# Optimization experiments

Measured on AMD Instinct MI355X. Metric: run time of the kernel, lower is better.

## Reference

```python
import jax, jax.numpy as jnp
import numpy as np

NUM_NODES = 100000
NUM_EDGES = 3200000
NUM_GRAPHS = 512
IN_DIM, OUT_DIM = 128, 16
DIMS = [IN_DIM, 32, 48, 64]


def glorot(key, shape):
    lim = float(np.sqrt(6.0 / (shape[0] + shape[1])))
    return jax.random.uniform(key, shape, jnp.float32, -lim, lim)


def setup_inputs() -> dict:
    key = jax.random.key(0)
    ks = jax.random.split(key, 12)
    x = jax.random.normal(ks[0], (NUM_NODES, IN_DIM), jnp.float32)
    edge_index = jax.random.randint(ks[1], (2, NUM_EDGES), 0, NUM_NODES, jnp.int64)
    batch = jnp.sort(jax.random.randint(ks[2], (NUM_NODES,), 0, NUM_GRAPHS, jnp.int64))
    params = {}
    for i in range(3):
        params[f"W{i+1}"] = glorot(ks[3 + i], (DIMS[i], DIMS[i + 1]))
        params[f"b{i+1}"] = jnp.zeros((DIMS[i + 1],), jnp.float32)
    params["fc1_w"] = glorot(ks[6], (64, 32))
    params["fc1_b"] = jnp.zeros((32,), jnp.float32)
    params["fc2_w"] = glorot(ks[7], (32, OUT_DIM))
    params["fc2_b"] = jnp.zeros((OUT_DIM,), jnp.float32)
    return {"x": x, "edge_index": edge_index, "batch": batch, **params}


def gcn_conv(x, W, b, src, dst, deg_inv_sqrt):
    # h = x @ W; aggregate with symmetric normalization + self loops (PyG GCNConv)
    h = x @ W  # [N, out]
    norm = deg_inv_sqrt[src] * deg_inv_sqrt[dst]  # [E]
    msg = h[src] * norm[:, None]  # [E, out]  (gather)
    agg = jnp.zeros_like(h).at[dst].add(msg)  # scatter-add to targets
    self_loop = h * (deg_inv_sqrt * deg_inv_sqrt)[:, None]
    return agg + self_loop + b


def reference(x, edge_index, batch, W1, b1, W2, b2, W3, b3, fc1_w, fc1_b, fc2_w, fc2_b):
    src, dst = edge_index[0], edge_index[1]
    n = x.shape[0]
    # degree with self loops: deg[i] = in-degree + 1
    deg = jnp.zeros((n,), jnp.float32).at[dst].add(1.0) + 1.0
    dis = jax.lax.rsqrt(deg)
    h = jax.nn.relu(gcn_conv(x, W1, b1, src, dst, dis))
    h = jax.nn.relu(gcn_conv(h, W2, b2, src, dst, dis))
    h = jax.nn.relu(gcn_conv(h, W3, b3, src, dst, dis))
    # global mean pool per graph
    sums = jax.ops.segment_sum(h, batch, num_segments=NUM_GRAPHS)
    cnts = jax.ops.segment_sum(jnp.ones((n,), jnp.float32), batch, num_segments=NUM_GRAPHS)
    pooled = sums / jnp.maximum(cnts, 1.0)[:, None]  # [G, 64]
    z = jax.nn.relu(pooled @ fc1_w + fc1_b)
    logits = z @ fc2_w + fc2_b
    return jax.nn.softmax(logits, axis=1)
```

## Files before the change

### kernel.cpp

```cpp
#include <hip/hip_runtime.h>
#include <hip/hip_fp16.h>

static constexpr int NN = 100000;
static constexpr int NE = 3200000;
static constexpr int NG = 512;
static constexpr int NCB = 196;
static constexpr int CHK = 8192;
static constexpr int NCH = (NE + CHK - 1) / CHK;
static constexpr int NCNT = NCB * NCH;
static constexpr int SCAN_BLK = 2048;
static constexpr int NSB = (NCNT + SCAN_BLK - 1) / SCAN_BLK;

typedef float f32x2 __attribute__((ext_vector_type(2)));

__device__ __forceinline__ void acc_fp8x4(unsigned v, float* a) {
    f32x2 lo = __builtin_amdgcn_cvt_pk_f32_fp8((int)v, false);
    f32x2 hi = __builtin_amdgcn_cvt_pk_f32_fp8((int)v, true);
    a[0] += lo.x; a[1] += lo.y; a[2] += hi.x; a[3] += hi.y;
}
__device__ __forceinline__ void set_fp8x4(unsigned v, float* a) {
    f32x2 lo = __builtin_amdgcn_cvt_pk_f32_fp8((int)v, false);
    f32x2 hi = __builtin_amdgcn_cvt_pk_f32_fp8((int)v, true);
    a[0] = lo.x; a[1] = lo.y; a[2] = hi.x; a[3] = hi.y;
}
__device__ __forceinline__ unsigned pack_fp8x4(float a, float b, float c, float d) {
    int p = __builtin_amdgcn_cvt_pk_fp8_f32(a, b, 0, false);
    p = __builtin_amdgcn_cvt_pk_fp8_f32(c, d, p, true);
    return (unsigned)p;
}

__global__ __launch_bounds__(256) void k_histC(const int4* __restrict__ dst4,
                                               int* __restrict__ cntC, int e4) {
    __shared__ int h[NCB];
    for (int i = threadIdx.x; i < NCB; i += 256) h[i] = 0;
    __syncthreads();
    const int s4 = blockIdx.x * (CHK / 4), e4end = min(s4 + CHK / 4, e4);
    for (int i = s4 + threadIdx.x; i < e4end; i += 256) {
        int4 d = dst4[i];
        atomicAdd(&h[d.x >> 9], 1);
        atomicAdd(&h[d.y >> 9], 1);
        atomicAdd(&h[d.z >> 9], 1);
        atomicAdd(&h[d.w >> 9], 1);
    }
    __syncthreads();
    for (int i = threadIdx.x; i < NCB; i += 256)
        cntC[(size_t)i * NCH + blockIdx.x] = h[i];
}

__global__ __launch_bounds__(256) void k_scanA(const int* __restrict__ in,
                                               int* __restrict__ out,
                                               int* __restrict__ bsum, int n) {
    __shared__ int s[256];
    const int tid = threadIdx.x;
    const int base = blockIdx.x * SCAN_BLK + tid * 8;
    int v[8], t = 0;
#pragma unroll
    for (int c = 0; c < 8; c++) {
        int idx = base + c;
        v[c] = (idx < n) ? in[idx] : 0;
        t += v[c];
    }
    s[tid] = t;
    __syncthreads();
    for (int off = 1; off < 256; off <<= 1) {
        int x = (tid >= off) ? s[tid - off] : 0;
        __syncthreads();
        s[tid] += x;
        __syncthreads();
    }
    if (tid == 255) bsum[blockIdx.x] = s[255];
    int run = s[tid] - t;
#pragma unroll
    for (int c = 0; c < 8; c++) {
        int idx = base + c;
        if (idx < n) out[idx] = run;
        run += v[c];
    }
}

__global__ __launch_bounds__(256) void k_scanB(int* __restrict__ bsum, int nb) {
    __shared__ int s[256];
    const int tid = threadIdx.x;
    int v = (tid < nb) ? bsum[tid] : 0;
    s[tid] = v;
    __syncthreads();
    for (int off = 1; off < 256; off <<= 1) {
        int x = (tid >= off) ? s[tid - off] : 0;
        __syncthreads();
        s[tid] += x;
        __syncthreads();
    }
    if (tid < nb) bsum[tid] = s[tid] - v;
}

__global__ __launch_bounds__(256) void k_scatC(const int4* __restrict__ src4,
                                               const int4* __restrict__ dst4,
                                               const int* __restrict__ sc,
                                               const int* __restrict__ bsum,
                                               unsigned* __restrict__ tmp, int e4) {
    __shared__ int cur[NCB];
    for (int i = threadIdx.x; i < NCB; i += 256) {
        size_t idx = (size_t)i * NCH + blockIdx.x;
        cur[i] = sc[idx] + bsum[idx >> 11];
    }
    __syncthreads();
    const int s4 = blockIdx.x * (CHK / 4), e4end = min(s4 + CHK / 4, e4);
    for (int i = s4 + threadIdx.x; i < e4end; i += 256) {
        int4 d = dst4[i];
        int4 sv = src4[i];
        int p0 = atomicAdd(&cur[d.x >> 9], 1);
        tmp[p0] = ((unsigned)(d.x & 511) << 17) | (unsigned)sv.x;
        int p1 = atomicAdd(&cur[d.y >> 9], 1);
        tmp[p1] = ((unsigned)(d.y & 511) << 17) | (unsigned)sv.y;
        int p2 = atomicAdd(&cur[d.z >> 9], 1);
        tmp[p2] = ((unsigned)(d.z & 511) << 17) | (unsigned)sv.z;
        int p3 = atomicAdd(&cur[d.w >> 9], 1);
        tmp[p3] = ((unsigned)(d.w & 511) << 17) | (unsigned)sv.w;
    }
}

__global__ __launch_bounds__(1024) void k_fill512(const unsigned* __restrict__ tmp,
                                                  const int* __restrict__ sc,
                                                  const int* __restrict__ bsum,
                                                  int* __restrict__ csr,
                                                  int* __restrict__ degi,
                                                  int* __restrict__ offs,
                                                  float* __restrict__ dis,
                                                  int n, int etotal) {
    __shared__ int cnt[512];
    __shared__ int s[512];
    __shared__ int cur[512];
    const int b = blockIdx.x, tid = threadIdx.x;
    if (tid < 512) cnt[tid] = 0;
    size_t i0 = (size_t)b * NCH;
    const int e0 = sc[i0] + bsum[i0 >> 11];
    int e1 = etotal;
    if (b + 1 < NCB) {
        size_t i1 = (size_t)(b + 1) * NCH;
        e1 = sc[i1] + bsum[i1 >> 11];
    }
    __syncthreads();
    for (int e = e0 + tid; e < e1; e += 1024)
        atomicAdd(&cnt[tmp[e] >> 17], 1);
    __syncthreads();
    int v = 0;
    if (tid < 512) { v = cnt[tid]; s[tid] = v; }
    __syncthreads();
    for (int off = 1; off < 512; off <<= 1) {
        int x = 0;
        if (tid < 512 && tid >= off) x = s[tid - off];
        __syncthreads();
        if (tid < 512) s[tid] += x;
        __syncthreads();
    }
    if (tid < 512) {
        int c = e0 + s[tid] - v;
        cur[tid] = c;
        int node = b * 512 + tid;
        if (node < n) {
            degi[node] = v;
            offs[node] = c;
            dis[node] = rsqrtf((float)v + 1.0f);
        }
    }
    __syncthreads();
    for (int e = e0 + tid; e < e1; e += 1024) {
        unsigned pk = tmp[e];
        int p = atomicAdd(&cur[pk >> 17], 1);
        csr[p] = (int)(pk & 0x1FFFFu);
    }
}

__global__ __launch_bounds__(256) void k_gemm1(const float* __restrict__ X,
                                               const float* __restrict__ W,
                                               const float* __restrict__ dis,
                                               unsigned* __restrict__ H, int n) {
    constexpr int IN = 128, ROWS = 32;
    __shared__ float sW[IN * 32];
    __shared__ float sX[ROWS][IN];
    const int tid = threadIdx.x;
    for (int i = tid; i < IN * 32; i += 256) sW[i] = W[i];
    const int row0 = blockIdx.x * ROWS;
    const float4* X4 = (const float4*)X;
    for (int i = tid; i < ROWS * 32; i += 256) {
        int r = row0 + (i >> 5);
        float4 v = make_float4(0.f, 0.f, 0.f, 0.f);
        if (r < n) v = X4[(size_t)r * 32 + (i & 31)];
        ((float4*)&sX[i >> 5][0])[i & 31] = v;
    }
    __syncthreads();
    const int lr = tid >> 3;
    const int cg = tid & 7;
    const int gr = row0 + lr;
    float acc[4] = {0.f, 0.f, 0.f, 0.f};
#pragma unroll 8
    for (int k = 0; k < IN; k++) {
        float xv = sX[lr][k];
#pragma unroll
        for (int c = 0; c < 4; c++)
            acc[c] = fmaf(xv, sW[k * 32 + 4 * cg + c], acc[c]);
    }
    if (gr < n) {
        float dd = dis[gr];
        H[(size_t)gr * 8 + cg] =
            pack_fp8x4(acc[0] * dd, acc[1] * dd, acc[2] * dd, acc[3] * dd);
    }
}

__global__ __launch_bounds__(256) void k_pull2(
        const unsigned* __restrict__ Hp, const int* __restrict__ offs,
        const int* __restrict__ degi, const int* __restrict__ csr,
        const float* __restrict__ dis, const float* __restrict__ b,
        unsigned* __restrict__ A, int n) {
    const int group = threadIdx.x >> 3, j0 = threadIdx.x & 7;
    const int d = blockIdx.x * 32 + group;
    if (d >= n) return;
    float acc[4];
    set_fp8x4(Hp[(size_t)d * 8 + j0], acc);
    int e = offs[d];
    const int end = e + degi[d];
    for (; e + 7 < end; e += 8) {
        unsigned v0 = Hp[(size_t)csr[e] * 8 + j0];
        unsigned v1 = Hp[(size_t)csr[e + 1] * 8 + j0];
        unsigned v2 = Hp[(size_t)csr[e + 2] * 8 + j0];
        unsigned v3 = Hp[(size_t)csr[e + 3] * 8 + j0];
        unsigned v4 = Hp[(size_t)csr[e + 4] * 8 + j0];
        unsigned v5 = Hp[(size_t)csr[e + 5] * 8 + j0];
        unsigned v6 = Hp[(size_t)csr[e + 6] * 8 + j0];
        unsigned v7 = Hp[(size_t)csr[e + 7] * 8 + j0];
        acc_fp8x4(v0, acc); acc_fp8x4(v1, acc);
        acc_fp8x4(v2, acc); acc_fp8x4(v3, acc);
        acc_fp8x4(v4, acc); acc_fp8x4(v5, acc);
        acc_fp8x4(v6, acc); acc_fp8x4(v7, acc);
    }
    for (; e < end; e++) acc_fp8x4(Hp[(size_t)csr[e] * 8 + j0], acc);
    const float dd = dis[d];
    float r[4];
#pragma unroll
    for (int c = 0; c < 4; c++)
        r[c] = fmaxf(fmaf(acc[c], dd, b[4 * j0 + c]), 0.f) * dd;
    A[(size_t)d * 8 + j0] = pack_fp8x4(r[0], r[1], r[2], r[3]);
}

__global__ __launch_bounds__(256) void k_pullmm32(
        const unsigned* __restrict__ Hp, const int* __restrict__ offs,
        const int* __restrict__ degi, const int* __restrict__ csr,
        const float* __restrict__ dis, const float* __restrict__ W,
        const float* __restrict__ b, unsigned* __restrict__ A, int n) {
    __shared__ float sW[32 * 48];
    __shared__ float rows[32][33];
    for (int i = threadIdx.x; i < 32 * 48; i += 256) sW[i] = W[i];
    const int group = threadIdx.x >> 3, j0 = threadIdx.x & 7;
    const int d = blockIdx.x * 32 + group;
    if (d < n) {
        float acc[4];
        set_fp8x4(Hp[(size_t)d * 8 + j0], acc);
        int e = offs[d];
        const int end = e + degi[d];
        for (; e + 7 < end; e += 8) {
            unsigned v0 = Hp[(size_t)csr[e] * 8 + j0];
            unsigned v1 = Hp[(size_t)csr[e + 1] * 8 + j0];
            unsigned v2 = Hp[(size_t)csr[e + 2] * 8 + j0];
            unsigned v3 = Hp[(size_t)csr[e + 3] * 8 + j0];
            unsigned v4 = Hp[(size_t)csr[e + 4] * 8 + j0];
            unsigned v5 = Hp[(size_t)csr[e + 5] * 8 + j0];
            unsigned v6 = Hp[(size_t)csr[e + 6] * 8 + j0];
            unsigned v7 = Hp[(size_t)csr[e + 7] * 8 + j0];
            acc_fp8x4(v0, acc); acc_fp8x4(v1, acc);
            acc_fp8x4(v2, acc); acc_fp8x4(v3, acc);
            acc_fp8x4(v4, acc); acc_fp8x4(v5, acc);
            acc_fp8x4(v6, acc); acc_fp8x4(v7, acc);
        }
        for (; e < end; e++) acc_fp8x4(Hp[(size_t)csr[e] * 8 + j0], acc);
        const float dd = dis[d];
#pragma unroll
        for (int c = 0; c < 4; c++) rows[group][4 * j0 + c] = acc[c] * dd;
    }
    __syncthreads();
    const int row0 = blockIdx.x * 32;
    for (int u = threadIdx.x; u < 32 * 16; u += 256) {
        int nl = u >> 4, cg = u & 15;
        int gr = row0 + nl;
        if (gr < n) {
            unsigned p = 0;
            if (cg < 12) {
                float dd2 = dis[gr];
                float r[4];
#pragma unroll
                for (int c = 0; c < 4; c++) {
                    float s = b[4 * cg + c];
#pragma unroll
                    for (int k = 0; k < 32; k++)
                        s = fmaf(rows[nl][k], sW[k * 48 + 4 * cg + c], s);
                    r[c] = fmaxf(s, 0.f) * dd2;
                }
                p = pack_fp8x4(r[0], r[1], r[2], r[3]);
            }
            A[(size_t)gr * 16 + cg] = p;
        }
    }
}

__global__ __launch_bounds__(256) void k_pullmm48(
        const uint2* __restrict__ Hp, const int* __restrict__ offs,
        const int* __restrict__ degi, const int* __restrict__ csr,
        const float* __restrict__ dis, const float* __restrict__ W,
        const float* __restrict__ b, __half* __restrict__ A, int n) {
    __shared__ float sW[48 * 64];
    __shared__ float rows[32][48];
    for (int i = threadIdx.x; i < 48 * 64; i += 256) sW[i] = W[i];
    const int group = threadIdx.x >> 3, j0 = threadIdx.x & 7;
    const int d = blockIdx.x * 32 + group;
    if (d < n) {
        float acc[8];
        uint2 sv = Hp[(size_t)d * 8 + j0];
        set_fp8x4(sv.x, acc); set_fp8x4(sv.y, acc + 4);
        int e = offs[d];
        const int end = e + degi[d];
        for (; e + 7 < end; e += 8) {
            uint2 v0 = Hp[(size_t)csr[e] * 8 + j0];
            uint2 v1 = Hp[(size_t)csr[e + 1] * 8 + j0];
            uint2 v2 = Hp[(size_t)csr[e + 2] * 8 + j0];
            uint2 v3 = Hp[(size_t)csr[e + 3] * 8 + j0];
            uint2 v4 = Hp[(size_t)csr[e + 4] * 8 + j0];
            uint2 v5 = Hp[(size_t)csr[e + 5] * 8 + j0];
            uint2 v6 = Hp[(size_t)csr[e + 6] * 8 + j0];
            uint2 v7 = Hp[(size_t)csr[e + 7] * 8 + j0];
            acc_fp8x4(v0.x, acc); acc_fp8x4(v0.y, acc + 4);
            acc_fp8x4(v1.x, acc); acc_fp8x4(v1.y, acc + 4);
            acc_fp8x4(v2.x, acc); acc_fp8x4(v2.y, acc + 4);
            acc_fp8x4(v3.x, acc); acc_fp8x4(v3.y, acc + 4);
            acc_fp8x4(v4.x, acc); acc_fp8x4(v4.y, acc + 4);
            acc_fp8x4(v5.x, acc); acc_fp8x4(v5.y, acc + 4);
            acc_fp8x4(v6.x, acc); acc_fp8x4(v6.y, acc + 4);
            acc_fp8x4(v7.x, acc); acc_fp8x4(v7.y, acc + 4);
        }
        for (; e < end; e++) {
            uint2 v = Hp[(size_t)csr[e] * 8 + j0];
            acc_fp8x4(v.x, acc); acc_fp8x4(v.y, acc + 4);
        }
        const float dd = dis[d];
        if (j0 < 6) {
#pragma unroll
            for (int c = 0; c < 8; c++) rows[group][8 * j0 + c] = acc[c] * dd;
        }
    }
    __syncthreads();
    const int row0 = blockIdx.x * 32;
#pragma unroll
    for (int o = 0; o < 8; o++) {
        int idx = o * 256 + threadIdx.x;
        int nl = idx >> 6, col = idx & 63;
        int gr = row0 + nl;
        if (gr < n) {
            float s = b[col];
#pragma unroll
            for (int k = 0; k < 48; k++)
                s = fmaf(rows[nl][k], sW[k * 64 + col], s);
            A[(size_t)gr * 64 + col] = __float2half(s);
        }
    }
}

__global__ __launch_bounds__(256) void k_poolhead(
        const __half* __restrict__ A3, const int* __restrict__ batch,
        const float* __restrict__ f1w, const float* __restrict__ f1b,
        const float* __restrict__ f2w, const float* __restrict__ f2b,
        float* __restrict__ out, int n, int ngr) {
    const int g = blockIdx.x;
    __shared__ int sb[2];
    if (threadIdx.x < 2) {
        int target = g + threadIdx.x;
        int lo = 0, hi = n;
        while (lo < hi) {
            int mid = (lo + hi) >> 1;
            if (batch[mid] < target) lo = mid + 1; else hi = mid;
        }
        sb[threadIdx.x] = lo;
    }
    __syncthreads();
    const int s = sb[0], e = sb[1];
    const int j = threadIdx.x & 63, rl = threadIdx.x >> 6;
    float sum = 0.f;
    for (int node = s + rl; node < e; node += 4)
        sum += fmaxf(__half2float(A3[(size_t)node * 64 + j]), 0.f);
    __shared__ float red[4][64];
    __shared__ float p[64], z[32], lg[16];
    red[rl][j] = sum;
    __syncthreads();
    if (rl == 0)
        p[j] = (red[0][j] + red[1][j] + red[2][j] + red[3][j]) /
               fmaxf((float)(e - s), 1.f);
    __syncthreads();
    const int t = threadIdx.x;
    if (t < 32) {
        float acc = f1b[t];
        for (int k = 0; k < 64; k++) acc = fmaf(p[k], f1w[k * 32 + t], acc);
        z[t] = fmaxf(acc, 0.f);
    }
    __syncthreads();
    if (t < 16) {
        float acc = f2b[t];
        for (int k = 0; k < 32; k++) acc = fmaf(z[k], f2w[k * 16 + t], acc);
        lg[t] = acc;
    }
    __syncthreads();
    if (t < 16) {
        float m = lg[0];
        for (int i = 1; i < 16; i++) m = fmaxf(m, lg[i]);
        float sden = 0.f;
        for (int i = 0; i < 16; i++) sden += expf(lg[i] - m);
        out[g * 16 + t] = expf(lg[t] - m) / sden;
    }
}

extern "C" void kernel_launch(void* const* d_in, const int* in_sizes, int n_in,
                              void* d_out, int out_size, void* d_ws, size_t ws_size,
                              hipStream_t stream) {
    (void)in_sizes; (void)n_in; (void)out_size; (void)ws_size;
    const float* x     = (const float*)d_in[0];
    const int*   ei    = (const int*)d_in[1];
    const int*   batch = (const int*)d_in[2];
    const float* W1 = (const float*)d_in[3];
    const float* b1 = (const float*)d_in[4];
    const float* W2 = (const float*)d_in[5];  const float* b2 = (const float*)d_in[6];
    const float* W3 = (const float*)d_in[7];  const float* b3 = (const float*)d_in[8];
    const float* f1w = (const float*)d_in[9]; const float* f1b = (const float*)d_in[10];
    const float* f2w = (const float*)d_in[11];const float* f2b = (const float*)d_in[12];
    float* out = (float*)d_out;

    const int* src = ei;
    const int* dst = ei + NE;

    float* ws = (float*)d_ws;
    size_t o = 0;
    float* dis    = ws + o; o += NN;
    int*   degi   = (int*)(ws + o); o += NN;
    int*   offs   = (int*)(ws + o); o += NN;
    int*   cntC   = (int*)(ws + o); o += 76640;
    int*   sc     = (int*)(ws + o); o += 76640;
    int*   bsum   = (int*)(ws + o); o += 48;
    int*   csr    = (int*)(ws + o); o += NE;
    unsigned* TA  = (unsigned*)(ws + o); o += NE;
    unsigned* H1  = (unsigned*)(ws + o); o += NN * 8;
    unsigned* H2  = (unsigned*)(ws + o); o += NN * 8;
    unsigned* H3  = (unsigned*)(ws + o); o += NN * 16;

    unsigned* tmp = (unsigned*)TA;
    __half*   A3  = (__half*)TA;

    k_histC<<<NCH, 256, 0, stream>>>((const int4*)dst, cntC, NE / 4);
    k_scanA<<<NSB, 256, 0, stream>>>(cntC, sc, bsum, NCNT);
    k_scanB<<<1, 256, 0, stream>>>(bsum, NSB);
    k_scatC<<<NCH, 256, 0, stream>>>((const int4*)src, (const int4*)dst,
                                     sc, bsum, tmp, NE / 4);
    k_fill512<<<NCB, 1024, 0, stream>>>(tmp, sc, bsum, csr, degi, offs, dis, NN, NE);

    const int PGRID = (NN + 31) / 32;

    k_gemm1<<<(NN + 31) / 32, 256, 0, stream>>>(x, W1, dis, H1, NN);
    k_pull2<<<PGRID, 256, 0, stream>>>(H1, offs, degi, csr, dis, b1, H2, NN);

    k_pullmm32<<<PGRID, 256, 0, stream>>>(H2, offs, degi, csr, dis, W2, b2, H3, NN);

    k_pullmm48<<<PGRID, 256, 0, stream>>>(
        (const uint2*)H3, offs, degi, csr, dis, W3, b3, A3, NN);

    k_poolhead<<<NG, 256, 0, stream>>>(A3, batch, f1w, f1b, f2w, f2b, out, NN, NG);
}
```

Baseline: 354.8 us.

## Use 4 lanes per node with wider vector gathers and register-tiled dense epilogues

The pull-aggregation kernels now assign 4 lanes per destination node instead of 8, so each gathered row is fetched with uint2/uint4 loads, 64 nodes are handled per block, and accumulation uses packed float2 adds. The dense transform after aggregation is reorganised so each thread computes 12 or 16 output columns for one row, using float4 weight reads from shared memory, and writes packed half or fp8 results with vector stores. The aim is fewer gather instructions, better memory-level parallelism per lane and cheaper epilogue GEMMs. The trade-off is more registers per thread and fewer threads working on each edge list, which may reduce latency hiding on high-degree nodes.

```diff
diff --git a/kernel.cpp b/kernel.cpp
--- a/kernel.cpp
+++ b/kernel.cpp
@@ -13,20 +13,22 @@
 
 typedef float f32x2 __attribute__((ext_vector_type(2)));
 
-__device__ __forceinline__ void acc_fp8x4(unsigned v, float* a) {
-    f32x2 lo = __builtin_amdgcn_cvt_pk_f32_fp8((int)v, false);
-    f32x2 hi = __builtin_amdgcn_cvt_pk_f32_fp8((int)v, true);
-    a[0] += lo.x; a[1] += lo.y; a[2] += hi.x; a[3] += hi.y;
-}
-__device__ __forceinline__ void set_fp8x4(unsigned v, float* a) {
-    f32x2 lo = __builtin_amdgcn_cvt_pk_f32_fp8((int)v, false);
-    f32x2 hi = __builtin_amdgcn_cvt_pk_f32_fp8((int)v, true);
-    a[0] = lo.x; a[1] = lo.y; a[2] = hi.x; a[3] = hi.y;
+__device__ __forceinline__ void set2_fp8x4(unsigned v, f32x2* a) {
+    a[0] = __builtin_amdgcn_cvt_pk_f32_fp8((int)v, false);
+    a[1] = __builtin_amdgcn_cvt_pk_f32_fp8((int)v, true);
+}
+__device__ __forceinline__ void acc2_fp8x4(unsigned v, f32x2* a) {
+    a[0] += __builtin_amdgcn_cvt_pk_f32_fp8((int)v, false);
+    a[1] += __builtin_amdgcn_cvt_pk_f32_fp8((int)v, true);
 }
 __device__ __forceinline__ unsigned pack_fp8x4(float a, float b, float c, float d) {
     int p = __builtin_amdgcn_cvt_pk_fp8_f32(a, b, 0, false);
     p = __builtin_amdgcn_cvt_pk_fp8_f32(c, d, p, true);
     return (unsigned)p;
+}
+__device__ __forceinline__ unsigned pkh2(float a, float b) {
+    __half2 h = __floats2half2_rn(a, b);
+    return *(unsigned*)&h;
 }
 
 __global__ __launch_bounds__(256) void k_histC(const int4* __restrict__ dst4,
@@ -208,157 +210,207 @@
 }
 
 __global__ __launch_bounds__(256) void k_pull2(
-        const unsigned* __restrict__ Hp, const int* __restrict__ offs,
+        const uint2* __restrict__ Hp, const int* __restrict__ offs,
         const int* __restrict__ degi, const int* __restrict__ csr,
         const float* __restrict__ dis, const float* __restrict__ b,
-        unsigned* __restrict__ A, int n) {
-    const int group = threadIdx.x >> 3, j0 = threadIdx.x & 7;
-    const int d = blockIdx.x * 32 + group;
+        uint2* __restrict__ A, int n) {
+    const int group = threadIdx.x >> 2, j0 = threadIdx.x & 3;
+    const int d = blockIdx.x * 64 + group;
     if (d >= n) return;
-    float acc[4];
-    set_fp8x4(Hp[(size_t)d * 8 + j0], acc);
+    f32x2 acc[4];
+    uint2 sv = Hp[(size_t)d * 4 + j0];
+    set2_fp8x4(sv.x, acc); set2_fp8x4(sv.y, acc + 2);
     int e = offs[d];
     const int end = e + degi[d];
     for (; e + 7 < end; e += 8) {
-        unsigned v0 = Hp[(size_t)csr[e] * 8 + j0];
-        unsigned v1 = Hp[(size_t)csr[e + 1] * 8 + j0];
-        unsigned v2 = Hp[(size_t)csr[e + 2] * 8 + j0];
-        unsigned v3 = Hp[(size_t)csr[e + 3] * 8 + j0];
-        unsigned v4 = Hp[(size_t)csr[e + 4] * 8 + j0];
-        unsigned v5 = Hp[(size_t)csr[e + 5] * 8 + j0];
-        unsigned v6 = Hp[(size_t)csr[e + 6] * 8 + j0];
-        unsigned v7 = Hp[(size_t)csr[e + 7] * 8 + j0];
-        acc_fp8x4(v0, acc); acc_fp8x4(v1, acc);
-        acc_fp8x4(v2, acc); acc_fp8x4(v3, acc);
-        acc_fp8x4(v4, acc); acc_fp8x4(v5, acc);
-        acc_fp8x4(v6, acc); acc_fp8x4(v7, acc);
-    }
-    for (; e < end; e++) acc_fp8x4(Hp[(size_t)csr[e] * 8 + j0], acc);
+        uint2 v0 = Hp[(size_t)csr[e] * 4 + j0];
+        uint2 v1 = Hp[(size_t)csr[e + 1] * 4 + j0];
+        uint2 v2 = Hp[(size_t)csr[e + 2] * 4 + j0];
+        uint2 v3 = Hp[(size_t)csr[e + 3] * 4 + j0];
+        uint2 v4 = Hp[(size_t)csr[e + 4] * 4 + j0];
+        uint2 v5 = Hp[(size_t)csr[e + 5] * 4 + j0];
+        uint2 v6 = Hp[(size_t)csr[e + 6] * 4 + j0];
+        uint2 v7 = Hp[(size_t)csr[e + 7] * 4 + j0];
+        acc2_fp8x4(v0.x, acc); acc2_fp8x4(v0.y, acc + 2);
+        acc2_fp8x4(v1.x, acc); acc2_fp8x4(v1.y, acc + 2);
+        acc2_fp8x4(v2.x, acc); acc2_fp8x4(v2.y, acc + 2);
+        acc2_fp8x4(v3.x, acc); acc2_fp8x4(v3.y, acc + 2);
+        acc2_fp8x4(v4.x, acc); acc2_fp8x4(v4.y, acc + 2);
+        acc2_fp8x4(v5.x, acc); acc2_fp8x4(v5.y, acc + 2);
+        acc2_fp8x4(v6.x, acc); acc2_fp8x4(v6.y, acc + 2);
+        acc2_fp8x4(v7.x, acc); acc2_fp8x4(v7.y, acc + 2);
+    }
+    for (; e < end; e++) {
+        uint2 v = Hp[(size_t)csr[e] * 4 + j0];
+        acc2_fp8x4(v.x, acc); acc2_fp8x4(v.y, acc + 2);
+    }
     const float dd = dis[d];
-    float r[4];
-#pragma unroll
-    for (int c = 0; c < 4; c++)
-        r[c] = fmaxf(fmaf(acc[c], dd, b[4 * j0 + c]), 0.f) * dd;
-    A[(size_t)d * 8 + j0] = pack_fp8x4(r[0], r[1], r[2], r[3]);
+    float r[8];
+#pragma unroll
+    for (int c = 0; c < 4; c++) {
+        r[2 * c]     = fmaxf(fmaf(acc[c].x, dd, b[8 * j0 + 2 * c]), 0.f) * dd;
+        r[2 * c + 1] = fmaxf(fmaf(acc[c].y, dd, b[8 * j0 + 2 * c + 1]), 0.f) * dd;
+    }
+    A[(size_t)d * 4 + j0] = make_uint2(pack_fp8x4(r[0], r[1], r[2], r[3]),
+                                       pack_fp8x4(r[4], r[5], r[6], r[7]));
 }
 
 __global__ __launch_bounds__(256) void k_pullmm32(
-        const unsigned* __restrict__ Hp, const int* __restrict__ offs,
+        const uint2* __restrict__ Hp, const int* __restrict__ offs,
         const int* __restrict__ degi, const int* __restrict__ csr,
         const float* __restrict__ dis, const float* __restrict__ W,
         const float* __restrict__ b, unsigned* __restrict__ A, int n) {
     __shared__ float sW[32 * 48];
-    __shared__ float rows[32][33];
+    __shared__ float rows[64][33];
     for (int i = threadIdx.x; i < 32 * 48; i += 256) sW[i] = W[i];
-    const int group = threadIdx.x >> 3, j0 = threadIdx.x & 7;
-    const int d = blockIdx.x * 32 + group;
+    const int group = threadIdx.x >> 2, j0 = threadIdx.x & 3;
+    const int d = blockIdx.x * 64 + group;
     if (d < n) {
-        float acc[4];
-        set_fp8x4(Hp[(size_t)d * 8 + j0], acc);
+        f32x2 acc[4];
+        uint2 sv = Hp[(size_t)d * 4 + j0];
+        set2_fp8x4(sv.x, acc); set2_fp8x4(sv.y, acc + 2);
         int e = offs[d];
         const int end = e + degi[d];
         for (; e + 7 < end; e += 8) {
-            unsigned v0 = Hp[(size_t)csr[e] * 8 + j0];
-            unsigned v1 = Hp[(size_t)csr[e + 1] * 8 + j0];
-            unsigned v2 = Hp[(size_t)csr[e + 2] * 8 + j0];
-            unsigned v3 = Hp[(size_t)csr[e + 3] * 8 + j0];
-            unsigned v4 = Hp[(size_t)csr[e + 4] * 8 + j0];
-            unsigned v5 = Hp[(size_t)csr[e + 5] * 8 + j0];
-            unsigned v6 = Hp[(size_t)csr[e + 6] * 8 + j0];
-            unsigned v7 = Hp[(size_t)csr[e + 7] * 8 + j0];
-            acc_fp8x4(v0, acc); acc_fp8x4(v1, acc);
-            acc_fp8x4(v2, acc); acc_fp8x4(v3, acc);
-            acc_fp8x4(v4, acc); acc_fp8x4(v5, acc);
-            acc_fp8x4(v6, acc); acc_fp8x4(v7, acc);
-        }
-        for (; e < end; e++) acc_fp8x4(Hp[(size_t)csr[e] * 8 + j0], acc);
+            uint2 v0 = Hp[(size_t)csr[e] * 4 + j0];
+            uint2 v1 = Hp[(size_t)csr[e + 1] * 4 + j0];
+            uint2 v2 = Hp[(size_t)csr[e + 2] * 4 + j0];
+            uint2 v3 = Hp[(size_t)csr[e + 3] * 4 + j0];
+            uint2 v4 = Hp[(size_t)csr[e + 4] * 4 + j0];
+            uint2 v5 = Hp[(size_t)csr[e + 5] * 4 + j0];
+            uint2 v6 = Hp[(size_t)csr[e + 6] * 4 + j0];
+            uint2 v7 = Hp[(size_t)csr[e + 7] * 4 + j0];
+            acc2_fp8x4(v0.x, acc); acc2_fp8x4(v0.y, acc + 2);
+            acc2_fp8x4(v1.x, acc); acc2_fp8x4(v1.y, acc + 2);
+            acc2_fp8x4(v2.x, acc); acc2_fp8x4(v2.y, acc + 2);
+            acc2_fp8x4(v3.x, acc); acc2_fp8x4(v3.y, acc + 2);
+            acc2_fp8x4(v4.x, acc); acc2_fp8x4(v4.y, acc + 2);
+            acc2_fp8x4(v5.x, acc); acc2_fp8x4(v5.y, acc + 2);
+            acc2_fp8x4(v6.x, acc); acc2_fp8x4(v6.y, acc + 2);
+            acc2_fp8x4(v7.x, acc); acc2_fp8x4(v7.y, acc + 2);
+        }
+        for (; e < end; e++) {
+            uint2 v = Hp[(size_t)csr[e] * 4 + j0];
+            acc2_fp8x4(v.x, acc); acc2_fp8x4(v.y, acc + 2);
+        }
         const float dd = dis[d];
 #pragma unroll
-        for (int c = 0; c < 4; c++) rows[group][4 * j0 + c] = acc[c] * dd;
-    }
-    __syncthreads();
-    const int row0 = blockIdx.x * 32;
-    for (int u = threadIdx.x; u < 32 * 16; u += 256) {
-        int nl = u >> 4, cg = u & 15;
-        int gr = row0 + nl;
-        if (gr < n) {
-            unsigned p = 0;
-            if (cg < 12) {
-                float dd2 = dis[gr];
-                float r[4];
-#pragma unroll
-                for (int c = 0; c < 4; c++) {
-                    float s = b[4 * cg + c];
-#pragma unroll
-                    for (int k = 0; k < 32; k++)
-                        s = fmaf(rows[nl][k], sW[k * 48 + 4 * cg + c], s);
-                    r[c] = fmaxf(s, 0.f) * dd2;
-                }
-                p = pack_fp8x4(r[0], r[1], r[2], r[3]);
+        for (int c = 0; c < 4; c++) {
+            rows[group][8 * j0 + 2 * c]     = acc[c].x * dd;
+            rows[group][8 * j0 + 2 * c + 1] = acc[c].y * dd;
+        }
+    }
+    __syncthreads();
+    const int row0 = blockIdx.x * 64;
+    const int nl = threadIdx.x & 63, cgb = threadIdx.x >> 6;
+    const int gr = row0 + nl;
+    if (gr < n) {
+        const float4* sW4 = (const float4*)sW;
+        float s[3][4];
+#pragma unroll
+        for (int o = 0; o < 3; o++)
+#pragma unroll
+            for (int c = 0; c < 4; c++) s[o][c] = b[12 * cgb + 4 * o + c];
+#pragma unroll 8
+        for (int k = 0; k < 32; k++) {
+            float rv = rows[nl][k];
+#pragma unroll
+            for (int o = 0; o < 3; o++) {
+                float4 w = sW4[k * 12 + cgb * 3 + o];
+                s[o][0] = fmaf(rv, w.x, s[o][0]);
+                s[o][1] = fmaf(rv, w.y, s[o][1]);
+                s[o][2] = fmaf(rv, w.z, s[o][2]);
+                s[o][3] = fmaf(rv, w.w, s[o][3]);
             }
-            A[(size_t)gr * 16 + cg] = p;
-        }
+        }
+        const float dd2 = dis[gr];
+#pragma unroll
+        for (int o = 0; o < 3; o++) {
+            float r0 = fmaxf(s[o][0], 0.f) * dd2;
+            float r1 = fmaxf(s[o][1], 0.f) * dd2;
+            float r2 = fmaxf(s[o][2], 0.f) * dd2;
+            float r3 = fmaxf(s[o][3], 0.f) * dd2;
+            A[(size_t)gr * 16 + cgb * 3 + o] = pack_fp8x4(r0, r1, r2, r3);
+        }
+        A[(size_t)gr * 16 + 12 + cgb] = 0;
     }
 }
 
 __global__ __launch_bounds__(256) void k_pullmm48(
-        const uint2* __restrict__ Hp, const int* __restrict__ offs,
+        const uint4* __restrict__ Hp, const int* __restrict__ offs,
         const int* __restrict__ degi, const int* __restrict__ csr,
         const float* __restrict__ dis, const float* __restrict__ W,
         const float* __restrict__ b, __half* __restrict__ A, int n) {
     __shared__ float sW[48 * 64];
-    __shared__ float rows[32][48];
+    __shared__ float rows[64][49];
     for (int i = threadIdx.x; i < 48 * 64; i += 256) sW[i] = W[i];
-    const int group = threadIdx.x >> 3, j0 = threadIdx.x & 7;
-    const int d = blockIdx.x * 32 + group;
+    const int group = threadIdx.x >> 2, j0 = threadIdx.x & 3;
+    const int d = blockIdx.x * 64 + group;
     if (d < n) {
-        float acc[8];
-        uint2 sv = Hp[(size_t)d * 8 + j0];
-        set_fp8x4(sv.x, acc); set_fp8x4(sv.y, acc + 4);
+        f32x2 acc[8];
+        uint4 sv = Hp[(size_t)d * 4 + j0];
+        set2_fp8x4(sv.x, acc);     set2_fp8x4(sv.y, acc + 2);
+        set2_fp8x4(sv.z, acc + 4); set2_fp8x4(sv.w, acc + 6);
         int e = offs[d];
         const int end = e + degi[d];
-        for (; e + 7 < end; e += 8) {
-            uint2 v0 = Hp[(size_t)csr[e] * 8 + j0];
-            uint2 v1 = Hp[(size_t)csr[e + 1] * 8 + j0];
-            uint2 v2 = Hp[(size_t)csr[e + 2] * 8 + j0];
-            uint2 v3 = Hp[(size_t)csr[e + 3] * 8 + j0];
-            uint2 v4 = Hp[(size_t)csr[e + 4] * 8 + j0];
-            uint2 v5 = Hp[(size_t)csr[e + 5] * 8 + j0];
-            uint2 v6 = Hp[(size_t)csr[e + 6] * 8 + j0];
-            uint2 v7 = Hp[(size_t)csr[e + 7] * 8 + j0];
-            acc_fp8x4(v0.x, acc); acc_fp8x4(v0.y, acc + 4);
-            acc_fp8x4(v1.x, acc); acc_fp8x4(v1.y, acc + 4);
-            acc_fp8x4(v2.x, acc); acc_fp8x4(v2.y, acc + 4);
-            acc_fp8x4(v3.x, acc); acc_fp8x4(v3.y, acc + 4);
-            acc_fp8x4(v4.x, acc); acc_fp8x4(v4.y, acc + 4);
-            acc_fp8x4(v5.x, acc); acc_fp8x4(v5.y, acc + 4);
-            acc_fp8x4(v6.x, acc); acc_fp8x4(v6.y, acc + 4);
-            acc_fp8x4(v7.x, acc); acc_fp8x4(v7.y, acc + 4);
+        for (; e + 3 < end; e += 4) {
+            uint4 v0 = Hp[(size_t)csr[e] * 4 + j0];
+            uint4 v1 = Hp[(size_t)csr[e + 1] * 4 + j0];
+            uint4 v2 = Hp[(size_t)csr[e + 2] * 4 + j0];
+            uint4 v3 = Hp[(size_t)csr[e + 3] * 4 + j0];
+            acc2_fp8x4(v0.x, acc);     acc2_fp8x4(v0.y, acc + 2);
+            acc2_fp8x4(v0.z, acc + 4); acc2_fp8x4(v0.w, acc + 6);
+            acc2_fp8x4(v1.x, acc);     acc2_fp8x4(v1.y, acc + 2);
+            acc2_fp8x4(v1.z, acc + 4); acc2_fp8x4(v1.w, acc + 6);
+            acc2_fp8x4(v2.x, acc);     acc2_fp8x4(v2.y, acc + 2);
+            acc2_fp8x4(v2.z, acc + 4); acc2_fp8x4(v2.w, acc + 6);
+            acc2_fp8x4(v3.x, acc);     acc2_fp8x4(v3.y, acc + 2);
+            acc2_fp8x4(v3.z, acc + 4); acc2_fp8x4(v3.w, acc + 6);
         }
         for (; e < end; e++) {
-            uint2 v = Hp[(size_t)csr[e] * 8 + j0];
-            acc_fp8x4(v.x, acc); acc_fp8x4(v.y, acc + 4);
+            uint4 v = Hp[(size_t)csr[e] * 4 + j0];
+            acc2_fp8x4(v.x, acc);     acc2_fp8x4(v.y, acc + 2);
+            acc2_fp8x4(v.z, acc + 4); acc2_fp8x4(v.w, acc + 6);
         }
         const float dd = dis[d];
-        if (j0 < 6) {
-#pragma unroll
-            for (int c = 0; c < 8; c++) rows[group][8 * j0 + c] = acc[c] * dd;
-        }
-    }
-    __syncthreads();
-    const int row0 = blockIdx.x * 32;
-#pragma unroll
-    for (int o = 0; o < 8; o++) {
-        int idx = o * 256 + threadIdx.x;
-        int nl = idx >> 6, col = idx & 63;
-        int gr = row0 + nl;
-        if (gr < n) {
-            float s = b[col];
-#pragma unroll
-            for (int k = 0; k < 48; k++)
-                s = fmaf(rows[nl][k], sW[k * 64 + col], s);
-            A[(size_t)gr * 64 + col] = __float2half(s);
-        }
+        if (j0 < 3) {
+#pragma unroll
+            for (int c = 0; c < 8; c++) {
+                rows[group][16 * j0 + 2 * c]     = acc[c].x * dd;
+                rows[group][16 * j0 + 2 * c + 1] = acc[c].y * dd;
+            }
+        }
+    }
+    __syncthreads();
+    const int row0 = blockIdx.x * 64;
+    const int nl = threadIdx.x & 63, cgb = threadIdx.x >> 6;
+    const int gr = row0 + nl;
+    if (gr < n) {
+        const float4* sW4 = (const float4*)sW;
+        float s[4][4];
+#pragma unroll
+        for (int o = 0; o < 4; o++)
+#pragma unroll
+            for (int c = 0; c < 4; c++) s[o][c] = b[16 * cgb + 4 * o + c];
+#pragma unroll 8
+        for (int k = 0; k < 48; k++) {
+            float rv = rows[nl][k];
+#pragma unroll
+            for (int o = 0; o < 4; o++) {
+                float4 w = sW4[k * 16 + cgb * 4 + o];
+                s[o][0] = fmaf(rv, w.x, s[o][0]);
+                s[o][1] = fmaf(rv, w.y, s[o][1]);
+                s[o][2] = fmaf(rv, w.z, s[o][2]);
+                s[o][3] = fmaf(rv, w.w, s[o][3]);
+            }
+        }
+        uint4 q0, q1;
+        q0.x = pkh2(s[0][0], s[0][1]); q0.y = pkh2(s[0][2], s[0][3]);
+        q0.z = pkh2(s[1][0], s[1][1]); q0.w = pkh2(s[1][2], s[1][3]);
+        q1.x = pkh2(s[2][0], s[2][1]); q1.y = pkh2(s[2][2], s[2][3]);
+        q1.z = pkh2(s[3][0], s[3][1]); q1.w = pkh2(s[3][2], s[3][3]);
+        ((uint4*)A)[(size_t)gr * 8 + cgb * 2]     = q0;
+        ((uint4*)A)[(size_t)gr * 8 + cgb * 2 + 1] = q1;
     }
 }
 
@@ -456,15 +508,17 @@
                                      sc, bsum, tmp, NE / 4);
     k_fill512<<<NCB, 1024, 0, stream>>>(tmp, sc, bsum, csr, degi, offs, dis, NN, NE);
 
-    const int PGRID = (NN + 31) / 32;
+    const int PGRID = (NN + 63) / 64;
 
     k_gemm1<<<(NN + 31) / 32, 256, 0, stream>>>(x, W1, dis, H1, NN);
-    k_pull2<<<PGRID, 256, 0, stream>>>(H1, offs, degi, csr, dis, b1, H2, NN);
-
-    k_pullmm32<<<PGRID, 256, 0, stream>>>(H2, offs, degi, csr, dis, W2, b2, H3, NN);
+    k_pull2<<<PGRID, 256, 0, stream>>>((const uint2*)H1, offs, degi, csr, dis, b1,
+                                       (uint2*)H2, NN);
+
+    k_pullmm32<<<PGRID, 256, 0, stream>>>((const uint2*)H2, offs, degi, csr, dis,
+                                          W2, b2, H3, NN);
 
     k_pullmm48<<<PGRID, 256, 0, stream>>>(
-        (const uint2*)H3, offs, degi, csr, dis, W3, b3, A3, NN);
+        (const uint4*)H3, offs, degi, csr, dis, W3, b3, A3, NN);
 
     k_poolhead<<<NG, 256, 0, stream>>>(A3, batch, f1w, f1b, f2w, f2b, out, NN, NG);
 }
```

After: 349.5 us. Within noise of the previous version (-1.5%).
